# Optimization experiments

Measured on AMD Instinct MI355X. Metric: run time of the kernel, lower is better.

## Reference

```python
import jax, jax.numpy as jnp
import numpy as np

V, T, E, H, L = 32000, 1024, 1024, 16, 6
D = E // H
FF = 4 * E
B = 2


def _ln(x, s, b, eps=1e-5):
    m = x.mean(-1, keepdims=True)
    v = x.var(-1, keepdims=True)
    return (x - m) * jax.lax.rsqrt(v + eps) * s + b


def setup_inputs() -> dict:
    key = jax.random.key(0)
    ks = jax.random.split(key, 16)
    std = 0.02
    inp = {
        "idx": jax.random.randint(ks[0], (B, T), 0, V),
        "tok_w": jax.random.normal(ks[1], (V, E)) * std,
        "pos_emb": jax.random.normal(ks[2], (1, T, E)) * std,
        # stacked per-layer params [L, ...]
        "ln1_s": jnp.ones((L, E)), "ln1_b": jnp.zeros((L, E)),
        "wq": jax.random.normal(ks[3], (L, E, E)) * std,
        "wk": jax.random.normal(ks[4], (L, E, E)) * std,
        "wv": jax.random.normal(ks[5], (L, E, E)) * std,
        "wo": jax.random.normal(ks[6], (L, E, E)) * std,
        "bo": jnp.zeros((L, E)),
        "ln2_s": jnp.ones((L, E)), "ln2_b": jnp.zeros((L, E)),
        "w1": jax.random.normal(ks[7], (L, E, FF)) * std,
        "b1": jnp.zeros((L, FF)),
        "w2": jax.random.normal(ks[8], (L, FF, E)) * std,
        "b2": jnp.zeros((L, E)),
        "lnf_s": jnp.ones((E,)), "lnf_b": jnp.zeros((E,)),
        "head_w": jax.random.normal(ks[9], (E, V)) * std,
        "head_b": jnp.zeros((V,)),
    }
    return inp


def _gpt(idx, tok_w, pos_emb, ln1_s, ln1_b, wq, wk, wv, wo, bo,
         ln2_s, ln2_b, w1, b1, w2, b2, lnf_s, lnf_b, head_w, head_b):
    x = tok_w[idx] + pos_emb[0, :T]                      # [B,T,E]
    mask = jnp.tril(jnp.ones((T, T), dtype=bool))        # causal mask
    scale = 1.0 / np.sqrt(D)

    def step(x, p):
        l1s, l1b, q_w, k_w, v_w, o_w, o_b, l2s, l2b, f1, fb1, f2, fb2 = p
        h = _ln(x, l1s, l1b)
        q = (h @ q_w).reshape(B, T, H, D)
        k = (h @ k_w).reshape(B, T, H, D)
        v = (h @ v_w).reshape(B, T, H, D)
        att = jnp.einsum('bthd,bshd->bhts', q, k) * scale  # [B,H,T,T]
        att = jnp.where(mask, att, -jnp.inf)
        att = jax.nn.softmax(att, axis=-1)
        o = jnp.einsum('bhts,bshd->bthd', att, v).reshape(B, T, E)
        x = x + o @ o_w + o_b
        h2 = _ln(x, l2s, l2b)
        x = x + jax.nn.relu(h2 @ f1 + fb1) @ f2 + fb2
        return x, None

    params = (ln1_s, ln1_b, wq, wk, wv, wo, bo, ln2_s, ln2_b, w1, b1, w2, b2)
    x, _ = jax.lax.scan(step, x, params)
    x = _ln(x, lnf_s, lnf_b)
    return x @ head_w + head_b                           # logits [B,T,V]


def reference(idx, tok_w, pos_emb, ln1_s, ln1_b, wq, wk, wv, wo, bo,
              ln2_s, ln2_b, w1, b1, w2, b2, lnf_s, lnf_b, head_w, head_b):
    return _gpt(idx, tok_w, pos_emb, ln1_s, ln1_b, wq, wk, wv, wo, bo,
                ln2_s, ln2_b, w1, b1, w2, b2, lnf_s, lnf_b, head_w, head_b)
```

## Files before the change

### kernel.cpp

```cpp
#include <hip/hip_runtime.h>


#define T_SEQ 1024
#define E_DIM 1024
#define H_NUM 16
#define D_HEAD 64
#define L_NUM 6
#define FF_DIM 4096
#define B_NUM 2
#define M_ROWS 2048

using bf16x8 = __attribute__((ext_vector_type(8))) __bf16;
using f32x4  = __attribute__((ext_vector_type(4))) float;

__device__ __forceinline__ unsigned short f2bf(float f) {
  unsigned int u = __float_as_uint(f);
  u += 0x7fffu + ((u >> 16) & 1u);
  return (unsigned short)(u >> 16);
}

__device__ __forceinline__ void gload_lds16(const void* g, void* l) {
  __builtin_amdgcn_global_load_lds(
      (const __attribute__((address_space(1))) unsigned int*)g,
      (__attribute__((address_space(3))) unsigned int*)l, 16, 0, 0);
}

__global__ __launch_bounds__(256) void embed_k(const int* __restrict__ idx,
                                               const float* __restrict__ tok_w,
                                               const float* __restrict__ pos,
                                               float* __restrict__ x) {
  const int i = blockIdx.x;
  const int t = i & (T_SEQ - 1);
  const int tok = idx[i];
  const float4 a = ((const float4*)(tok_w + (size_t)tok * E_DIM))[threadIdx.x];
  const float4 p = ((const float4*)(pos + (size_t)t * E_DIM))[threadIdx.x];
  float4 o;
  o.x = a.x + p.x; o.y = a.y + p.y; o.z = a.z + p.z; o.w = a.w + p.w;
  ((float4*)(x + (size_t)i * E_DIM))[threadIdx.x] = o;
}

__global__ __launch_bounds__(256) void ln_k(const float* __restrict__ x,
                                            const float* __restrict__ s,
                                            const float* __restrict__ b,
                                            unsigned short* __restrict__ out) {
  const int row = blockIdx.x, tid = threadIdx.x;
  const float4 v = ((const float4*)(x + (size_t)row * E_DIM))[tid];
  float sum = v.x + v.y + v.z + v.w;
  float sq  = v.x * v.x + v.y * v.y + v.z * v.z + v.w * v.w;
  #pragma unroll
  for (int off = 32; off; off >>= 1) {
    sum += __shfl_down(sum, off);
    sq  += __shfl_down(sq, off);
  }
  __shared__ float sm[10];
  const int wave = tid >> 6, lane = tid & 63;
  if (lane == 0) { sm[wave] = sum; sm[4 + wave] = sq; }
  __syncthreads();
  if (tid == 0) {
    const float ts = sm[0] + sm[1] + sm[2] + sm[3];
    const float tq = sm[4] + sm[5] + sm[6] + sm[7];
    const float mean = ts * (1.0f / E_DIM);
    const float var = tq * (1.0f / E_DIM) - mean * mean;
    sm[8] = mean;
    sm[9] = 1.0f / sqrtf(var + 1e-5f);
  }
  __syncthreads();
  const float mean = sm[8], inv = sm[9];
  const float4 sv = ((const float4*)s)[tid];
  const float4 bv = ((const float4*)b)[tid];
  ushort4 o;
  o.x = f2bf((v.x - mean) * inv * sv.x + bv.x);
  o.y = f2bf((v.y - mean) * inv * sv.y + bv.y);
  o.z = f2bf((v.z - mean) * inv * sv.z + bv.z);
  o.w = f2bf((v.w - mean) * inv * sv.w + bv.w);
  *(ushort4*)(out + (size_t)row * E_DIM + (tid << 2)) = o;
}

__global__ __launch_bounds__(256) void transpose_k(const float* __restrict__ W,
                                                   unsigned short* __restrict__ WT,
                                                   int K, int ldw) {
  __shared__ float tile[32][33];
  const int n0 = blockIdx.x << 5, k0 = blockIdx.y << 5;
  const int tx = threadIdx.x & 31, ty = threadIdx.x >> 5;
  #pragma unroll
  for (int i = ty; i < 32; i += 8)
    tile[i][tx] = W[(size_t)(k0 + i) * ldw + n0 + tx];
  __syncthreads();
  #pragma unroll
  for (int i = ty; i < 32; i += 8)
    WT[(size_t)(n0 + i) * K + k0 + tx] = f2bf(tile[tx][i]);
}

template<int BM, bool RELU, bool BIAS, bool RES, bool OBF16>
__global__ __launch_bounds__(256) void gemm_k(const unsigned short* __restrict__ A,
                                              const unsigned short* __restrict__ WT,
                                              const float* __restrict__ bias,
                                              const float* __restrict__ res,
                                              void* __restrict__ Cout,
                                              int ldc, int K) {
  constexpr int BN = 128;
  constexpr int BK = 64;
  constexpr int MF = BM / 32;
  constexpr int AJ = (BM * BK * 2 / 1024) / 4;
  constexpr int BJ = (BN * BK * 2 / 1024) / 4;
  __shared__ __align__(16) unsigned short As[2][BM][BK];
  __shared__ __align__(16) unsigned short Bs[2][BN][BK];
  const int tid = threadIdx.x;
  const int row0 = blockIdx.x * BM, col0 = blockIdx.y * BN;
  const int wave = tid >> 6, lane = tid & 63;
  const int wm = (wave >> 1) * (BM / 2), wn = (wave & 1) * 64;
  const int lr = lane & 15, lg = lane >> 4;
  const int ric = lane >> 3;
  const int sslot = lane & 7;

  auto stage = [&](int buf, int k0) {
    #pragma unroll
    for (int j = 0; j < AJ; ++j) {
      const int c = wave + 4 * j;
      const int row = c * 8 + ric;
      const int sp = sslot ^ (row & 7);
      gload_lds16(A + (size_t)(row0 + row) * K + k0 + sp * 8,
                  (char*)&As[buf][0][0] + c * 1024);
    }
    #pragma unroll
    for (int j = 0; j < BJ; ++j) {
      const int c = wave + 4 * j;
      const int row = c * 8 + ric;
      const int sp = sslot ^ (row & 7);
      gload_lds16(WT + (size_t)(col0 + row) * K + k0 + sp * 8,
                  (char*)&Bs[buf][0][0] + c * 1024);
    }
  };

  f32x4 acc[MF][4] = {};
  const int nt = K / BK;
  stage(0, 0);
  __syncthreads();
  for (int t = 0; t < nt; ++t) {
    const int cur = t & 1;
    if (t + 1 < nt) stage(cur ^ 1, (t + 1) * BK);
    #pragma unroll
    for (int ks = 0; ks < 2; ++ks) {
      bf16x8 af[MF], bfr[4];
      #pragma unroll
      for (int m = 0; m < MF; ++m) {
        const int r = wm + m * 16 + lr;
        const int s = (ks * 4 + lg) ^ (r & 7);
        af[m] = *(const bf16x8*)((const char*)&As[cur][0][0] + r * 128 + s * 16);
      }
      #pragma unroll
      for (int n = 0; n < 4; ++n) {
        const int r = wn + n * 16 + lr;
        const int s = (ks * 4 + lg) ^ (r & 7);
        bfr[n] = *(const bf16x8*)((const char*)&Bs[cur][0][0] + r * 128 + s * 16);
      }
      #pragma unroll
      for (int m = 0; m < MF; ++m)
        #pragma unroll
        for (int n = 0; n < 4; ++n)
          acc[m][n] = __builtin_amdgcn_mfma_f32_16x16x32_bf16(af[m], bfr[n], acc[m][n], 0, 0, 0);
    }
    __syncthreads();
  }
  float* Cf = (float*)Cout;
  unsigned short* Cb = (unsigned short*)Cout;
  #pragma unroll
  for (int m = 0; m < MF; ++m) {
    #pragma unroll
    for (int n = 0; n < 4; ++n) {
      const int col = col0 + wn + (n << 4) + lr;
      const float bv = BIAS ? bias[col] : 0.0f;
      #pragma unroll
      for (int r = 0; r < 4; ++r) {
        const int row = row0 + wm + (m << 4) + (lg << 2) + r;
        float val = acc[m][n][r] + bv;
        if (RELU) val = fmaxf(val, 0.0f);
        if (RES)  val += res[(size_t)row * ldc + col];
        if (OBF16) Cb[(size_t)row * ldc + col] = f2bf(val);
        else       Cf[(size_t)row * ldc + col] = val;
      }
    }
  }
}

#define QBLK 64
#define KBLK 64
__global__ __launch_bounds__(256) void fattn_k(const unsigned short* __restrict__ qkv,
                                               unsigned short* __restrict__ ob) {
  const int qt = blockIdx.x, h = blockIdx.y, b = blockIdx.z;
  const int tid = threadIdx.x;
  const int wave = tid >> 6, lane = tid & 63;
  const int lr = lane & 15, lg = lane >> 4;
  const int q0 = qt * QBLK;

  __shared__ __align__(16) unsigned short Qs[QBLK][72];
  __shared__ __align__(16) unsigned short Ks[KBLK][72];
  __shared__ __align__(16) unsigned short Vt[D_HEAD][72];
  __shared__ __align__(16) unsigned short Ps[QBLK][72];

  const size_t base = (size_t)b * T_SEQ * 3072 + (size_t)h * 64;
  const int srow = tid >> 3, scol = (tid & 7) << 3;

  #pragma unroll
  for (int it = 0; it < 2; ++it) {
    const int row = srow + it * 32;
    *(uint4*)&Qs[row][scol] =
        *(const uint4*)(qkv + base + (size_t)(q0 + row) * 3072 + scol);
  }
  __syncthreads();
  bf16x8 qf[2];
  #pragma unroll
  for (int ks = 0; ks < 2; ++ks)
    qf[ks] = *(const bf16x8*)&Qs[wave * 16 + lr][ks * 32 + lg * 8];

  f32x4 acc_o[4] = {};
  float mrow[4], lrow[4];
  #pragma unroll
  for (int r = 0; r < 4; ++r) { mrow[r] = -3.0e38f; lrow[r] = 0.f; }

  const int ntile = qt + 1;
  for (int kt = 0; kt < ntile; ++kt) {
    const int s0 = kt * KBLK;
    __syncthreads();
    #pragma unroll
    for (int it = 0; it < 2; ++it) {
      const int row = srow + it * 32;
      *(uint4*)&Ks[row][scol] =
          *(const uint4*)(qkv + base + 1024 + (size_t)(s0 + row) * 3072 + scol);
      uint4 v4 = *(const uint4*)(qkv + base + 2048 + (size_t)(s0 + row) * 3072 + scol);
      const unsigned short* vs = (const unsigned short*)&v4;
      #pragma unroll
      for (int j = 0; j < 8; ++j) Vt[scol + j][row] = vs[j];
    }
    __syncthreads();

    f32x4 sacc[4] = {};
    #pragma unroll
    for (int ks = 0; ks < 2; ++ks) {
      #pragma unroll
      for (int nf = 0; nf < 4; ++nf) {
        bf16x8 kf = *(const bf16x8*)&Ks[nf * 16 + lr][ks * 32 + lg * 8];
        sacc[nf] = __builtin_amdgcn_mfma_f32_16x16x32_bf16(qf[ks], kf, sacc[nf], 0, 0, 0);
      }
    }
    float sv[4][4];
    #pragma unroll
    for (int nf = 0; nf < 4; ++nf)
      #pragma unroll
      for (int r = 0; r < 4; ++r) sv[nf][r] = sacc[nf][r] * 0.125f;
    if (kt == ntile - 1) {
      #pragma unroll
      for (int nf = 0; nf < 4; ++nf) {
        const int s = s0 + nf * 16 + lr;
        #pragma unroll
        for (int r = 0; r < 4; ++r) {
          const int q = q0 + wave * 16 + lg * 4 + r;
          if (s > q) sv[nf][r] = -3.0e38f;
        }
      }
    }
    float p[4][4];
    #pragma unroll
    for (int r = 0; r < 4; ++r) {
      float mx = fmaxf(fmaxf(sv[0][r], sv[1][r]), fmaxf(sv[2][r], sv[3][r]));
      #pragma unroll
      for (int off = 1; off < 16; off <<= 1) mx = fmaxf(mx, __shfl_xor(mx, off));
      const float mnew = fmaxf(mrow[r], mx);
      const float alpha = __expf(mrow[r] - mnew);
      mrow[r] = mnew;
      float sum = 0.f;
      #pragma unroll
      for (int nf = 0; nf < 4; ++nf) {
        p[nf][r] = __expf(sv[nf][r] - mnew);
        sum += p[nf][r];
      }
      #pragma unroll
      for (int off = 1; off < 16; off <<= 1) sum += __shfl_xor(sum, off);
      lrow[r] = lrow[r] * alpha + sum;
      #pragma unroll
      for (int df = 0; df < 4; ++df) acc_o[df][r] *= alpha;
    }
    #pragma unroll
    for (int nf = 0; nf < 4; ++nf)
      #pragma unroll
      for (int r = 0; r < 4; ++r)
        Ps[wave * 16 + lg * 4 + r][nf * 16 + lr] = f2bf(p[nf][r]);
    __syncthreads();
    #pragma unroll
    for (int ks = 0; ks < 2; ++ks) {
      bf16x8 pa = *(const bf16x8*)&Ps[wave * 16 + lr][ks * 32 + lg * 8];
      #pragma unroll
      for (int df = 0; df < 4; ++df) {
        bf16x8 vf = *(const bf16x8*)&Vt[df * 16 + lr][ks * 32 + lg * 8];
        acc_o[df] = __builtin_amdgcn_mfma_f32_16x16x32_bf16(pa, vf, acc_o[df], 0, 0, 0);
      }
    }
  }
  #pragma unroll
  for (int r = 0; r < 4; ++r) {
    const float inv = 1.0f / lrow[r];
    const int row = q0 + wave * 16 + lg * 4 + r;
    #pragma unroll
    for (int df = 0; df < 4; ++df)
      ob[((size_t)b * T_SEQ + row) * E_DIM + h * 64 + df * 16 + lr] =
          f2bf(acc_o[df][r] * inv);
  }
}

extern "C" void kernel_launch(void* const* d_in, const int* in_sizes, int n_in,
                              void* d_out, int out_size, void* d_ws, size_t ws_size,
                              hipStream_t stream) {
  (void)in_sizes; (void)n_in; (void)out_size; (void)ws_size;
  const int*   idx    = (const int*)d_in[0];
  const float* tok_w  = (const float*)d_in[1];
  const float* pos    = (const float*)d_in[2];
  const float* ln1_s  = (const float*)d_in[3];
  const float* ln1_b  = (const float*)d_in[4];
  const float* wq     = (const float*)d_in[5];
  const float* wk     = (const float*)d_in[6];
  const float* wv     = (const float*)d_in[7];
  const float* wo     = (const float*)d_in[8];
  const float* bo     = (const float*)d_in[9];
  const float* ln2_s  = (const float*)d_in[10];
  const float* ln2_b  = (const float*)d_in[11];
  const float* w1     = (const float*)d_in[12];
  const float* b1     = (const float*)d_in[13];
  const float* w2     = (const float*)d_in[14];
  const float* b2     = (const float*)d_in[15];
  const float* lnf_s  = (const float*)d_in[16];
  const float* lnf_b  = (const float*)d_in[17];
  const float* head_w = (const float*)d_in[18];
  const float* head_b = (const float*)d_in[19];
  float* out = (float*)d_out;

  char* p = (char*)d_ws;
  float* x            = (float*)p;          p += (size_t)M_ROWS * E_DIM * 4;
  unsigned short* qkvb= (unsigned short*)p; p += (size_t)M_ROWS * 3072 * 4;
  unsigned short* h   = (unsigned short*)p; p += (size_t)M_ROWS * E_DIM * 2;
  unsigned short* obuf= (unsigned short*)p; p += (size_t)M_ROWS * E_DIM * 2;
  unsigned short* ff  = (unsigned short*)p; p += (size_t)M_ROWS * FF_DIM * 2;
  unsigned short* wt  = (unsigned short*)p; p += (size_t)32000 * E_DIM * 2;

  embed_k<<<M_ROWS, 256, 0, stream>>>(idx, tok_w, pos, x);

  for (int l = 0; l < L_NUM; ++l) {
    const size_t lEE = (size_t)l * E_DIM * E_DIM;
    const size_t lEF = (size_t)l * E_DIM * FF_DIM;
    ln_k<<<M_ROWS, 256, 0, stream>>>(x, ln1_s + l * E_DIM, ln1_b + l * E_DIM, h);
    transpose_k<<<dim3(32, 32), 256, 0, stream>>>(wq + lEE, wt,               E_DIM, E_DIM);
    transpose_k<<<dim3(32, 32), 256, 0, stream>>>(wk + lEE, wt + 1048576,     E_DIM, E_DIM);
    transpose_k<<<dim3(32, 32), 256, 0, stream>>>(wv + lEE, wt + 2097152,     E_DIM, E_DIM);
    gemm_k<128,false,false,false,true><<<dim3(16, 24), 256, 0, stream>>>(
        h, wt, nullptr, nullptr, qkvb, 3072, E_DIM);
    fattn_k<<<dim3(T_SEQ / QBLK, H_NUM, B_NUM), 256, 0, stream>>>(qkvb, obuf);
    transpose_k<<<dim3(32, 32), 256, 0, stream>>>(wo + lEE, wt, E_DIM, E_DIM);
    gemm_k<64,false,true,true,false><<<dim3(32, 8), 256, 0, stream>>>(
        obuf, wt, bo + l * E_DIM, x, x, E_DIM, E_DIM);
    ln_k<<<M_ROWS, 256, 0, stream>>>(x, ln2_s + l * E_DIM, ln2_b + l * E_DIM, h);
    transpose_k<<<dim3(128, 32), 256, 0, stream>>>(w1 + lEF, wt, E_DIM, FF_DIM);
    gemm_k<128,true,true,false,true><<<dim3(16, 32), 256, 0, stream>>>(
        h, wt, b1 + l * FF_DIM, nullptr, ff, FF_DIM, E_DIM);
    transpose_k<<<dim3(32, 128), 256, 0, stream>>>(w2 + lEF, wt, FF_DIM, E_DIM);
    gemm_k<64,false,true,true,false><<<dim3(32, 8), 256, 0, stream>>>(
        ff, wt, b2 + l * E_DIM, x, x, E_DIM, FF_DIM);
  }

  ln_k<<<M_ROWS, 256, 0, stream>>>(x, lnf_s, lnf_b, h);
  transpose_k<<<dim3(1000, 32), 256, 0, stream>>>(head_w, wt, E_DIM, 32000);
  gemm_k<128,false,true,false,false><<<dim3(16, 250), 256, 0, stream>>>(
      h, wt, head_b, nullptr, out, 32000, E_DIM);
}
```

Baseline: 1.525 ms.

## Batch weight transposes up front and use larger 512-thread GEMM tiles

All per-layer weight transposes/bf16 conversions move out of the layer loop into seven batched launches that write separate per-layer transposed buffers. This cuts launch count and keeps the transposed weights resident instead of reusing one scratch buffer. The GEMM is generalized to configurable block and warp tiling, so the QKV, FF1 and head GEMMs now use 128x256 or 256x256 tiles with 8 waves. The inner loop is reordered to preload the B fragments and to raise wave priority around the MFMA bursts. The cost is a much larger workspace and more LDS per block, which may lower occupancy.

Result: slower. 1.663 ms (+9.0%).

```diff
diff --git a/kernel.cpp b/kernel.cpp
--- a/kernel.cpp
+++ b/kernel.cpp
@@ -76,55 +76,56 @@
   *(ushort4*)(out + (size_t)row * E_DIM + (tid << 2)) = o;
 }
 
-__global__ __launch_bounds__(256) void transpose_k(const float* __restrict__ W,
+__global__ __launch_bounds__(256) void transpose_b(const float* __restrict__ W,
                                                    unsigned short* __restrict__ WT,
-                                                   int K, int ldw) {
+                                                   int K, int N,
+                                                   size_t Wstride, size_t WTstride) {
   __shared__ float tile[32][33];
+  const int z = blockIdx.z;
+  W  += (size_t)z * Wstride;
+  WT += (size_t)z * WTstride;
   const int n0 = blockIdx.x << 5, k0 = blockIdx.y << 5;
   const int tx = threadIdx.x & 31, ty = threadIdx.x >> 5;
   #pragma unroll
   for (int i = ty; i < 32; i += 8)
-    tile[i][tx] = W[(size_t)(k0 + i) * ldw + n0 + tx];
+    tile[i][tx] = W[(size_t)(k0 + i) * N + n0 + tx];
   __syncthreads();
   #pragma unroll
   for (int i = ty; i < 32; i += 8)
     WT[(size_t)(n0 + i) * K + k0 + tx] = f2bf(tile[tx][i]);
 }
 
-template<int BM, bool RELU, bool BIAS, bool RES, bool OBF16>
-__global__ __launch_bounds__(256) void gemm_k(const unsigned short* __restrict__ A,
-                                              const unsigned short* __restrict__ WT,
-                                              const float* __restrict__ bias,
-                                              const float* __restrict__ res,
-                                              void* __restrict__ Cout,
-                                              int ldc, int K) {
-  constexpr int BN = 128;
+template<int BM, int BN, int NW, int WM, int WN,
+         bool RELU, bool BIAS, bool RES, bool OBF16>
+__global__ __launch_bounds__(NW * 64) void gemm_s(
+    const unsigned short* __restrict__ A, const unsigned short* __restrict__ WT,
+    const float* __restrict__ bias, const float* __restrict__ res,
+    void* __restrict__ Cout, int ldc, int K) {
   constexpr int BK = 64;
-  constexpr int MF = BM / 32;
-  constexpr int AJ = (BM * BK * 2 / 1024) / 4;
-  constexpr int BJ = (BN * BK * 2 / 1024) / 4;
+  constexpr int WTM = BM / WM, WTN = BN / WN;
+  constexpr int MR = WTM / 16, NR = WTN / 16;
+  constexpr int ACH = BM / 8, BCH = BN / 8;
   __shared__ __align__(16) unsigned short As[2][BM][BK];
   __shared__ __align__(16) unsigned short Bs[2][BN][BK];
   const int tid = threadIdx.x;
   const int row0 = blockIdx.x * BM, col0 = blockIdx.y * BN;
   const int wave = tid >> 6, lane = tid & 63;
-  const int wm = (wave >> 1) * (BM / 2), wn = (wave & 1) * 64;
+  const int wm = (wave / WN) * WTM, wn = (wave % WN) * WTN;
   const int lr = lane & 15, lg = lane >> 4;
-  const int ric = lane >> 3;
-  const int sslot = lane & 7;
+  const int ric = lane >> 3, sslot = lane & 7;
 
   auto stage = [&](int buf, int k0) {
     #pragma unroll
-    for (int j = 0; j < AJ; ++j) {
-      const int c = wave + 4 * j;
+    for (int j = 0; j < ACH / NW; ++j) {
+      const int c = wave + NW * j;
       const int row = c * 8 + ric;
       const int sp = sslot ^ (row & 7);
       gload_lds16(A + (size_t)(row0 + row) * K + k0 + sp * 8,
                   (char*)&As[buf][0][0] + c * 1024);
     }
     #pragma unroll
-    for (int j = 0; j < BJ; ++j) {
-      const int c = wave + 4 * j;
+    for (int j = 0; j < BCH / NW; ++j) {
+      const int c = wave + NW * j;
       const int row = c * 8 + ric;
       const int sp = sslot ^ (row & 7);
       gload_lds16(WT + (size_t)(col0 + row) * K + k0 + sp * 8,
@@ -132,47 +133,49 @@
     }
   };
 
-  f32x4 acc[MF][4] = {};
+  f32x4 acc[MR][NR] = {};
   const int nt = K / BK;
   stage(0, 0);
   __syncthreads();
   for (int t = 0; t < nt; ++t) {
     const int cur = t & 1;
     if (t + 1 < nt) stage(cur ^ 1, (t + 1) * BK);
-    #pragma unroll
-    for (int ks = 0; ks < 2; ++ks) {
-      bf16x8 af[MF], bfr[4];
-      #pragma unroll
-      for (int m = 0; m < MF; ++m) {
-        const int r = wm + m * 16 + lr;
-        const int s = (ks * 4 + lg) ^ (r & 7);
-        af[m] = *(const bf16x8*)((const char*)&As[cur][0][0] + r * 128 + s * 16);
-      }
-      #pragma unroll
-      for (int n = 0; n < 4; ++n) {
+    bf16x8 bfr[NR][2];
+    #pragma unroll
+    for (int n = 0; n < NR; ++n)
+      #pragma unroll
+      for (int ks = 0; ks < 2; ++ks) {
         const int r = wn + n * 16 + lr;
         const int s = (ks * 4 + lg) ^ (r & 7);
-        bfr[n] = *(const bf16x8*)((const char*)&Bs[cur][0][0] + r * 128 + s * 16);
-      }
-      #pragma unroll
-      for (int m = 0; m < MF; ++m)
-        #pragma unroll
-        for (int n = 0; n < 4; ++n)
-          acc[m][n] = __builtin_amdgcn_mfma_f32_16x16x32_bf16(af[m], bfr[n], acc[m][n], 0, 0, 0);
+        bfr[n][ks] = *(const bf16x8*)((const char*)&Bs[cur][0][0] + r * 128 + s * 16);
+      }
+    #pragma unroll
+    for (int m = 0; m < MR; ++m) {
+      const int r = wm + m * 16 + lr;
+      const bf16x8 af0 = *(const bf16x8*)((const char*)&As[cur][0][0] + r * 128 + ((0 + lg) ^ (r & 7)) * 16);
+      const bf16x8 af1 = *(const bf16x8*)((const char*)&As[cur][0][0] + r * 128 + ((4 + lg) ^ (r & 7)) * 16);
+      __builtin_amdgcn_s_setprio(1);
+      #pragma unroll
+      for (int n = 0; n < NR; ++n)
+        acc[m][n] = __builtin_amdgcn_mfma_f32_16x16x32_bf16(af0, bfr[n][0], acc[m][n], 0, 0, 0);
+      #pragma unroll
+      for (int n = 0; n < NR; ++n)
+        acc[m][n] = __builtin_amdgcn_mfma_f32_16x16x32_bf16(af1, bfr[n][1], acc[m][n], 0, 0, 0);
+      __builtin_amdgcn_s_setprio(0);
     }
     __syncthreads();
   }
   float* Cf = (float*)Cout;
   unsigned short* Cb = (unsigned short*)Cout;
   #pragma unroll
-  for (int m = 0; m < MF; ++m) {
-    #pragma unroll
-    for (int n = 0; n < 4; ++n) {
-      const int col = col0 + wn + (n << 4) + lr;
+  for (int m = 0; m < MR; ++m) {
+    #pragma unroll
+    for (int n = 0; n < NR; ++n) {
+      const int col = col0 + wn + n * 16 + lr;
       const float bv = BIAS ? bias[col] : 0.0f;
       #pragma unroll
       for (int r = 0; r < 4; ++r) {
-        const int row = row0 + wm + (m << 4) + (lg << 2) + r;
+        const int row = row0 + wm + m * 16 + lg * 4 + r;
         float val = acc[m][n][r] + bv;
         if (RELU) val = fmaxf(val, 0.0f);
         if (RES)  val += res[(size_t)row * ldc + col];
@@ -335,38 +338,53 @@
 
   char* p = (char*)d_ws;
   float* x            = (float*)p;          p += (size_t)M_ROWS * E_DIM * 4;
-  unsigned short* qkvb= (unsigned short*)p; p += (size_t)M_ROWS * 3072 * 4;
+  unsigned short* qkvb= (unsigned short*)p; p += (size_t)M_ROWS * 3072 * 2;
   unsigned short* h   = (unsigned short*)p; p += (size_t)M_ROWS * E_DIM * 2;
   unsigned short* obuf= (unsigned short*)p; p += (size_t)M_ROWS * E_DIM * 2;
   unsigned short* ff  = (unsigned short*)p; p += (size_t)M_ROWS * FF_DIM * 2;
-  unsigned short* wt  = (unsigned short*)p; p += (size_t)32000 * E_DIM * 2;
+  unsigned short* wtqkv=(unsigned short*)p; p += (size_t)L_NUM * 3072 * E_DIM * 2;
+  unsigned short* wto = (unsigned short*)p; p += (size_t)L_NUM * E_DIM * E_DIM * 2;
+  unsigned short* wt1 = (unsigned short*)p; p += (size_t)L_NUM * FF_DIM * E_DIM * 2;
+  unsigned short* wt2 = (unsigned short*)p; p += (size_t)L_NUM * E_DIM * FF_DIM * 2;
+  unsigned short* wth = (unsigned short*)p; p += (size_t)32000 * E_DIM * 2;
+
+  transpose_b<<<dim3(32, 32, L_NUM), 256, 0, stream>>>(
+      wq, wtqkv,           E_DIM, E_DIM, (size_t)E_DIM * E_DIM, (size_t)3072 * E_DIM);
+  transpose_b<<<dim3(32, 32, L_NUM), 256, 0, stream>>>(
+      wk, wtqkv + 1048576, E_DIM, E_DIM, (size_t)E_DIM * E_DIM, (size_t)3072 * E_DIM);
+  transpose_b<<<dim3(32, 32, L_NUM), 256, 0, stream>>>(
+      wv, wtqkv + 2097152, E_DIM, E_DIM, (size_t)E_DIM * E_DIM, (size_t)3072 * E_DIM);
+  transpose_b<<<dim3(32, 32, L_NUM), 256, 0, stream>>>(
+      wo, wto, E_DIM, E_DIM, (size_t)E_DIM * E_DIM, (size_t)E_DIM * E_DIM);
+  transpose_b<<<dim3(128, 32, L_NUM), 256, 0, stream>>>(
+      w1, wt1, E_DIM, FF_DIM, (size_t)E_DIM * FF_DIM, (size_t)FF_DIM * E_DIM);
+  transpose_b<<<dim3(32, 128, L_NUM), 256, 0, stream>>>(
+      w2, wt2, FF_DIM, E_DIM, (size_t)E_DIM * FF_DIM, (size_t)E_DIM * FF_DIM);
+  transpose_b<<<dim3(1000, 32, 1), 256, 0, stream>>>(
+      head_w, wth, E_DIM, 32000, 0, 0);
 
   embed_k<<<M_ROWS, 256, 0, stream>>>(idx, tok_w, pos, x);
 
   for (int l = 0; l < L_NUM; ++l) {
-    const size_t lEE = (size_t)l * E_DIM * E_DIM;
-    const size_t lEF = (size_t)l * E_DIM * FF_DIM;
     ln_k<<<M_ROWS, 256, 0, stream>>>(x, ln1_s + l * E_DIM, ln1_b + l * E_DIM, h);
-    transpose_k<<<dim3(32, 32), 256, 0, stream>>>(wq + lEE, wt,               E_DIM, E_DIM);
-    transpose_k<<<dim3(32, 32), 256, 0, stream>>>(wk + lEE, wt + 1048576,     E_DIM, E_DIM);
-    transpose_k<<<dim3(32, 32), 256, 0, stream>>>(wv + lEE, wt + 2097152,     E_DIM, E_DIM);
-    gemm_k<128,false,false,false,true><<<dim3(16, 24), 256, 0, stream>>>(
-        h, wt, nullptr, nullptr, qkvb, 3072, E_DIM);
+    gemm_s<128, 256, 8, 2, 4, false, false, false, true>
+        <<<dim3(16, 12), 512, 0, stream>>>(
+        h, wtqkv + (size_t)l * 3072 * E_DIM, nullptr, nullptr, qkvb, 3072, E_DIM);
     fattn_k<<<dim3(T_SEQ / QBLK, H_NUM, B_NUM), 256, 0, stream>>>(qkvb, obuf);
-    transpose_k<<<dim3(32, 32), 256, 0, stream>>>(wo + lEE, wt, E_DIM, E_DIM);
-    gemm_k<64,false,true,true,false><<<dim3(32, 8), 256, 0, stream>>>(
-        obuf, wt, bo + l * E_DIM, x, x, E_DIM, E_DIM);
+    gemm_s<64, 128, 4, 2, 2, false, true, true, false>
+        <<<dim3(32, 8), 256, 0, stream>>>(
+        obuf, wto + (size_t)l * E_DIM * E_DIM, bo + l * E_DIM, x, x, E_DIM, E_DIM);
     ln_k<<<M_ROWS, 256, 0, stream>>>(x, ln2_s + l * E_DIM, ln2_b + l * E_DIM, h);
-    transpose_k<<<dim3(128, 32), 256, 0, stream>>>(w1 + lEF, wt, E_DIM, FF_DIM);
-    gemm_k<128,true,true,false,true><<<dim3(16, 32), 256, 0, stream>>>(
-        h, wt, b1 + l * FF_DIM, nullptr, ff, FF_DIM, E_DIM);
-    transpose_k<<<dim3(32, 128), 256, 0, stream>>>(w2 + lEF, wt, FF_DIM, E_DIM);
-    gemm_k<64,false,true,true,false><<<dim3(32, 8), 256, 0, stream>>>(
-        ff, wt, b2 + l * E_DIM, x, x, E_DIM, FF_DIM);
+    gemm_s<128, 256, 8, 2, 4, true, true, false, true>
+        <<<dim3(16, 16), 512, 0, stream>>>(
+        h, wt1 + (size_t)l * FF_DIM * E_DIM, b1 + l * FF_DIM, nullptr, ff, FF_DIM, E_DIM);
+    gemm_s<64, 128, 4, 2, 2, false, true, true, false>
+        <<<dim3(32, 8), 256, 0, stream>>>(
+        ff, wt2 + (size_t)l * E_DIM * FF_DIM, b2 + l * E_DIM, x, x, E_DIM, FF_DIM);
   }
 
   ln_k<<<M_ROWS, 256, 0, stream>>>(x, lnf_s, lnf_b, h);
-  transpose_k<<<dim3(1000, 32), 256, 0, stream>>>(head_w, wt, E_DIM, 32000);
-  gemm_k<128,false,true,false,false><<<dim3(16, 250), 256, 0, stream>>>(
-      h, wt, head_b, nullptr, out, 32000, E_DIM);
-}
+  gemm_s<256, 256, 8, 2, 4, false, true, false, false>
+      <<<dim3(8, 125), 512, 0, stream>>>(
+      h, wth, head_b, nullptr, out, 32000, E_DIM);
+}
```
